# Performance work log

Measured on AMD Instinct MI355X. Metric: run time of the kernel, lower is better.

Reference implementation:

```python
import jax, jax.numpy as jnp
import numpy as np

NEIGH = 16  # default neigh in __init__


def setup_inputs() -> dict:
    key = jax.random.key(0)
    kx, kuv = jax.random.split(key)
    B, M = 8, 4096
    X = jax.random.normal(kx, (B, M, 3), dtype=jnp.float32)
    uv = jax.random.uniform(kuv, (B, M, 2), dtype=jnp.float32)
    return {"X": X, "uv": uv}


def reference(X, uv):
    # Pairwise squared distances in parameter (uv) space: (B, M, M)
    dm = jnp.sum((uv[:, :, None, :] - uv[:, None, :, :]) ** 2, axis=-1)
    # k nearest neighbours (smallest distances) -> indices (B, M, K)
    _, k_inds = jax.lax.top_k(-dm, NEIGH)
    # Gather 3D neighbourhoods: (B, M, K, 3)
    knns = jax.vmap(lambda x, idx: x[idx])(X, k_inds)
    # Covariance per point: center then K x 3 outer products -> (B, M, 3, 3)
    centered = knns - jnp.mean(knns, axis=2, keepdims=True)
    cov = jnp.einsum('bmki,bmkj->bmij', centered, centered)
    # Symmetric 3x3 eigenvalues; torch sorts descending, eigvalsh is ascending
    eig = jnp.linalg.eigvalsh(cov)
    fff = eig[..., ::-1]  # (B, M, 3), descending
    return fff
```

## Files before the change

### kernel.cpp

```cpp
#include <hip/hip_runtime.h>
#include <math.h>

typedef unsigned long long u64;
typedef unsigned int u32;

constexpr int NB  = 8;
constexpr int NM  = 4096;
constexpr int KNN = 16;
constexpr int WPB = 8;
constexpr int QPW = 4;
constexpr int QPB = WPB * QPW;
constexpr int BLK = WPB * 64;
constexpr int GC  = 32;
constexpr int NC  = GC * GC;
constexpr int CSST = NC + 1;
constexpr int SLG = 13;

constexpr size_t WS_UVS = 0;
constexpr size_t WS_CS  = (size_t)NB * NM * 16;

__device__ __forceinline__ u64 shflx64(u64 v, int m) {
  unsigned lo = (unsigned)v, hi = (unsigned)(v >> 32);
  lo = __shfl_xor(lo, m, 64);
  hi = __shfl_xor(hi, m, 64);
  return ((u64)hi << 32) | lo;
}
__device__ __forceinline__ int rfl(int x) { return __builtin_amdgcn_readfirstlane(x); }
__device__ __forceinline__ int lanes_below(u64 m) {
  return (int)__builtin_amdgcn_mbcnt_hi((u32)(m >> 32),
             __builtin_amdgcn_mbcnt_lo((u32)m, 0u));
}
__device__ __forceinline__ u32 gm16(u64 m, int lane) {
  return (u32)(m >> ((lane >> 4) << 4)) & 0xFFFFu;
}

__global__ __launch_bounds__(1024)
void bin_pts(const float* __restrict__ uv, float4* __restrict__ uvS,
             u32* __restrict__ cs) {
  __shared__ u32 cnt[NC];
  __shared__ u32 offs[NC];
  __shared__ u32 wtot[16];
  const int bb  = blockIdx.x;
  const int tid = threadIdx.x;

  cnt[tid] = 0;
  __syncthreads();

  float2 c4[4];
  int cell[4];
  #pragma unroll
  for (int i = 0; i < 4; ++i) {
    const int p = tid + i * 1024;
    const float2 c = ((const float2*)(uv + (size_t)bb * NM * 2))[p];
    int cx = (int)(c.x * 32.f); cx = cx > GC - 1 ? GC - 1 : (cx < 0 ? 0 : cx);
    int cy = (int)(c.y * 32.f); cy = cy > GC - 1 ? GC - 1 : (cy < 0 ? 0 : cy);
    c4[i] = c; cell[i] = cy * GC + cx;
    atomicAdd(&cnt[cell[i]], 1u);
  }
  __syncthreads();

  {
    const int lane = tid & 63;
    u32 inc = cnt[tid];
    #pragma unroll
    for (int o = 1; o < 64; o <<= 1) {
      const u32 t = __shfl_up(inc, o, 64);
      if (lane >= o) inc += t;
    }
    offs[tid] = inc;
    if (lane == 63) wtot[tid >> 6] = inc;
  }
  __syncthreads();
  if (tid < 16) {
    u32 v = wtot[tid];
    #pragma unroll
    for (int o = 1; o < 16; o <<= 1) {
      const u32 t = __shfl_up(v, o, 64);
      if (tid >= o) v += t;
    }
    wtot[tid] = v;
  }
  __syncthreads();
  {
    const int w = tid >> 6;
    const u32 base = w ? wtot[w - 1] : 0u;
    const u32 excl = base + offs[tid] - cnt[tid];
    cs[bb * CSST + tid] = excl;
    offs[tid] = excl;
    if (tid == 0) cs[bb * CSST + NC] = NM;
  }
  __syncthreads();

  #pragma unroll
  for (int i = 0; i < 4; ++i) {
    const int p = tid + i * 1024;
    const u32 pos = atomicAdd(&offs[cell[i]], 1u);
    uvS[(size_t)bb * NM + pos] =
        make_float4(c4[i].x, c4[i].y, __uint_as_float((u32)p), 0.f);
  }
}

__global__ __launch_bounds__(BLK, 8)
void knn_eig(const float* __restrict__ X, const float4* __restrict__ uvS,
             const u32* __restrict__ cs, float* __restrict__ out) {
  __shared__ u64 surv[WPB][QPW * 32];

  const int tid  = threadIdx.x;
  const int lane = tid & 63;
  const int sub  = lane & 15;
  const int g4   = lane >> 4;
  const int wv   = tid >> 6;
  const int bb   = blockIdx.x >> 7;
  const int s    = ((blockIdx.x & 127) << 5) + (wv << 2) + g4;

  const float4* uvb = uvS + (size_t)bb * NM;
  const u32* csb = cs + bb * CSST;

  const float4 qc = uvb[s];
  const float qu = qc.x, qv = qc.y;
  const u32 oq = __float_as_uint(qc.z);
  int cxv = (int)(qu * 32.f); cxv = cxv > GC - 1 ? GC - 1 : (cxv < 0 ? 0 : cxv);
  int cyv = (int)(qv * 32.f); cyv = cyv > GC - 1 ? GC - 1 : (cyv < 0 ? 0 : cyv);
  const int sx = (qu * 32.f - (float)cxv >= 0.5f) ? 1 : 0;
  const int sy = (qv * 32.f - (float)cyv >= 0.5f) ? 1 : 0;

  float d[SLG];
  #pragma unroll
  for (int t = 0; t < SLG; ++t) d[t] = 1e30f;

  constexpr float TAU1 = 0.0017f;
  constexpr float TAU2 = 0.002197265625f;
  constexpr float TAU3 = 0.006103515625f;
  constexpr float TAU4 = 0.019775390625f;

  int rs0, rs1, rs2, rs3, rs4, rs5, rc0, rc1, rc2, rc3, rc4;
  int total, tsw;
  int cnt = 0;

  {
    const int x0 = min(max(cxv - 2 + sx, 0), GC - 4);
    const int y0 = min(max(cyv - 2 + sy, 0), GC - 4);
    const int b = y0 * GC + x0;
    rs0 = (int)csb[b];          rc0 = (int)csb[b + 4] - rs0;
    rs1 = (int)csb[b + GC];     rc1 = rc0 + (int)csb[b + GC + 4] - rs1;
    rs2 = (int)csb[b + 2*GC];   rc2 = rc1 + (int)csb[b + 2*GC + 4] - rs2;
    rs3 = (int)csb[b + 3*GC];   total = rc2 + (int)csb[b + 3*GC + 4] - rs3;
    rc3 = total; rc4 = total; rs4 = 0; rs5 = 0;
    int ts = min((total + 15) >> 4, SLG);
    int m1 = max(ts, __shfl_xor(ts, 16, 64));
    m1 = max(m1, __shfl_xor(m1, 32, 64));
    tsw = rfl(m1);
    #pragma unroll
    for (int t = 0; t < SLG; ++t) {
      if (t >= tsw) break;
      const int L = t * 16 + sub;
      int addr = rs0 + L;
      addr = (L >= rc0) ? rs1 + (L - rc0) : addr;
      addr = (L >= rc1) ? rs2 + (L - rc1) : addr;
      addr = (L >= rc2) ? rs3 + (L - rc2) : addr;
      float dd = 1e30f;
      if (L < total) {
        const float4 c = uvb[addr];
        const float dx = __fsub_rn(qu, c.x);
        const float dy = __fsub_rn(qv, c.y);
        dd = __fadd_rn(__fmul_rn(dx, dx), __fmul_rn(dy, dy));
      }
      d[t] = dd;
      cnt += (int)__popc(gm16(__ballot(dd <= TAU1), lane));
    }
  }

  float hi2 = TAU1, lo = 0.f;
  if (__any(cnt < KNN)) {
    int c2 = 0;
    #pragma unroll
    for (int t = 0; t < SLG; ++t) {
      if (t >= tsw) break;
      c2 += (int)__popc(gm16(__ballot(d[t] <= TAU2), lane));
    }
    if (cnt < KNN) { lo = TAU1; hi2 = TAU2; cnt = c2; }
  }

  if (__any(cnt < KNN)) {
    const bool need = cnt < KNN;
    int ts2 = 0;
    if (need) {
      #pragma unroll
      for (int t = 0; t < SLG; ++t) d[t] = 1e30f;
      const int x0 = min(max(cxv - 3 + sx, 0), GC - 6);
      const int y0 = min(max(cyv - 3 + sy, 0), GC - 6);
      const int b = y0 * GC + x0;
      rs0 = (int)csb[b];          rc0 = (int)csb[b + 6] - rs0;
      rs1 = (int)csb[b + GC];     rc1 = rc0 + (int)csb[b + GC + 6] - rs1;
      rs2 = (int)csb[b + 2*GC];   rc2 = rc1 + (int)csb[b + 2*GC + 6] - rs2;
      rs3 = (int)csb[b + 3*GC];   rc3 = rc2 + (int)csb[b + 3*GC + 6] - rs3;
      rs4 = (int)csb[b + 4*GC];   rc4 = rc3 + (int)csb[b + 4*GC + 6] - rs4;
      rs5 = (int)csb[b + 5*GC];   total = rc4 + (int)csb[b + 5*GC + 6] - rs5;
      ts2 = min((total + 15) >> 4, SLG);
      lo = TAU2; hi2 = TAU3;
    }
    int m1 = max(ts2, __shfl_xor(ts2, 16, 64));
    m1 = max(m1, __shfl_xor(m1, 32, 64));
    const int tsw2 = rfl(m1);
    int c2 = 0;
    #pragma unroll
    for (int t = 0; t < SLG; ++t) {
      if (t >= tsw2) break;
      float dd = 1e30f;
      if (need) {
        const int L = t * 16 + sub;
        int addr = rs0 + L;
        addr = (L >= rc0) ? rs1 + (L - rc0) : addr;
        addr = (L >= rc1) ? rs2 + (L - rc1) : addr;
        addr = (L >= rc2) ? rs3 + (L - rc2) : addr;
        addr = (L >= rc3) ? rs4 + (L - rc3) : addr;
        addr = (L >= rc4) ? rs5 + (L - rc4) : addr;
        if (L < total) {
          const float4 c = uvb[addr];
          const float dx = __fsub_rn(qu, c.x);
          const float dy = __fsub_rn(qv, c.y);
          dd = __fadd_rn(__fmul_rn(dx, dx), __fmul_rn(dy, dy));
        }
        d[t] = dd;
      }
      c2 += (int)__popc(gm16(__ballot(dd <= TAU3), lane));
    }
    if (need) cnt = c2;
    tsw = max(tsw, tsw2);
  }

  for (int it = 0; __any(cnt > 32) && it < 40; ++it) {
    const float mid = 0.5f * (lo + hi2);
    int c = 0;
    #pragma unroll
    for (int t = 0; t < SLG; ++t) {
      if (t >= tsw) break;
      c += (int)__popc(gm16(__ballot((cnt > 32) && (d[t] <= mid)), lane));
    }
    if (cnt > 32) {
      if (!(mid > lo && mid < hi2)) cnt = 32;
      else if (c >= KNN) { hi2 = mid; cnt = c; }
      else lo = mid;
    }
  }

  u64* sb = surv[wv];
  {
    int base = 0;
    #pragma unroll
    for (int t = 0; t < SLG; ++t) {
      if (t >= tsw) break;
      const bool p = d[t] <= hi2;
      const u32 mg = gm16(__ballot(p), lane);
      if (p) {
        const int pos = base + (int)__popc(mg & ((1u << sub) - 1u));
        if (pos < 32) {
          const int L = t * 16 + sub;
          int addr = rs0 + L;
          addr = (L >= rc0) ? rs1 + (L - rc0) : addr;
          addr = (L >= rc1) ? rs2 + (L - rc1) : addr;
          addr = (L >= rc2) ? rs3 + (L - rc2) : addr;
          addr = (L >= rc3) ? rs4 + (L - rc3) : addr;
          addr = (L >= rc4) ? rs5 + (L - rc4) : addr;
          const u32 oid = ((const u32*)(uvb + addr))[2];
          sb[(g4 << 5) + pos] = ((u64)__float_as_uint(d[t]) << 32) | (u64)oid;
        }
      }
      base += (int)__popc(mg);
    }
  }

  if (__any(cnt < KNN)) {
    #pragma unroll 1
    for (int g = 0; g < QPW; ++g) {
      if (!rfl((__shfl(cnt, g << 4, 64) < KNN) ? 1 : 0)) continue;
      const float gu = __shfl(qu, g << 4, 64);
      const float gv = __shfl(qv, g << 4, 64);
      int gcx = (int)(gu * 32.f); gcx = min(max(gcx, 0), GC - 1);
      int gcy = (int)(gv * 32.f); gcy = min(max(gcy, 0), GC - 1);
      const int gsx = (gu * 32.f - (float)gcx >= 0.5f) ? 1 : 0;
      const int gsy = (gv * 32.f - (float)gcy >= 0.5f) ? 1 : 0;
      const int x0 = min(max(gcx - 5 + gsx, 0), GC - 10);
      const int y0 = min(max(gcy - 5 + gsy, 0), GC - 10);
      int rstart[10], rcum[10];
      int cum = 0;
      #pragma unroll
      for (int r = 0; r < 10; ++r) {
        const int b = (y0 + r) * GC + x0;
        rstart[r] = (int)csb[b];
        cum += (int)csb[b + 10] - rstart[r];
        rcum[r] = cum;
      }
      const int gtotal = cum;
      const int gts = rfl(min((gtotal + 63) >> 6, SLG));
      float ghi = TAU4, glo = TAU3;
      int gcnt = 0;
      #pragma unroll
      for (int t = 0; t < SLG; ++t) {
        if (t >= gts) break;
        const int L = t * 64 + lane;
        int addr = rstart[0] + L;
        #pragma unroll
        for (int r = 1; r < 10; ++r)
          addr = (L >= rcum[r - 1]) ? rstart[r] + (L - rcum[r - 1]) : addr;
        float dd = 1e30f;
        if (L < gtotal) {
          const float4 c = uvb[addr];
          const float dx = __fsub_rn(gu, c.x);
          const float dy = __fsub_rn(gv, c.y);
          dd = __fadd_rn(__fmul_rn(dx, dx), __fmul_rn(dy, dy));
        }
        d[t] = dd;
        gcnt += (int)__popcll(__ballot(dd <= ghi));
      }
      for (int it = 0; rfl(gcnt) > 32 && it < 40; ++it) {
        const float mid = 0.5f * (glo + ghi);
        if (!(mid > glo && mid < ghi)) break;
        int c = 0;
        #pragma unroll
        for (int t = 0; t < SLG; ++t) {
          if (t >= gts) break;
          c += (int)__popcll(__ballot(d[t] <= mid));
        }
        if (c >= KNN) { ghi = mid; gcnt = c; } else glo = mid;
      }
      int base = 0;
      #pragma unroll
      for (int t = 0; t < SLG; ++t) {
        if (t >= gts) break;
        const bool p = d[t] <= ghi;
        const u64 m = __ballot(p);
        if (p) {
          const int pos = base + lanes_below(m);
          if (pos < 32) {
            const int L = t * 64 + lane;
            int addr = rstart[0] + L;
            #pragma unroll
            for (int r = 1; r < 10; ++r)
              addr = (L >= rcum[r - 1]) ? rstart[r] + (L - rcum[r - 1]) : addr;
            const u32 oid = ((const u32*)(uvb + addr))[2];
            sb[(g << 5) + pos] = ((u64)__float_as_uint(d[t]) << 32) | (u64)oid;
          }
        }
        base += (int)__popcll(m);
      }
      if (g4 == g) cnt = min(rfl(gcnt), 32);
    }
  }

  const int S = cnt < 32 ? cnt : 32;
  const int sbase = g4 << 5;
  u64 v0 = (sub < S) ? sb[sbase + sub] : ~0ull;
  u64 v1 = (16 + sub < S) ? sb[sbase + 16 + sub] : ~0ull;
  #pragma unroll
  for (int k = 2; k <= 16; k <<= 1) {
    #pragma unroll
    for (int j = k >> 1; j > 0; j >>= 1) {
      const u64 o0 = shflx64(v0, j);
      const u64 o1 = shflx64(v1, j);
      const bool up = ((sub & k) == 0);
      const bool j0 = ((sub & j) == 0);
      const bool km0 = (j0 == up);
      const bool km1 = (j0 != up);
      v0 = ((v0 < o0) == km0) ? v0 : o0;
      v1 = ((v1 < o1) == km1) ? v1 : o1;
    }
  }
  const u64 v = (v0 < v1) ? v0 : v1;

  const int idx = (int)(u32)v & 0xFFF;
  const float* Xp = X + ((size_t)bb * NM + idx) * 3;
  const float x = Xp[0], y = Xp[1], z = Xp[2];
  float sxs = x, sys = y, szs = z;
  float sxx = x * x, sxy = x * y, sxz = x * z;
  float syy = y * y, syz = y * z, szz = z * z;
  #pragma unroll
  for (int o = 8; o > 0; o >>= 1) {
    sxs += __shfl_xor(sxs, o, 64);  sys += __shfl_xor(sys, o, 64);
    szs += __shfl_xor(szs, o, 64);  sxx += __shfl_xor(sxx, o, 64);
    sxy += __shfl_xor(sxy, o, 64);  sxz += __shfl_xor(sxz, o, 64);
    syy += __shfl_xor(syy, o, 64);  syz += __shfl_xor(syz, o, 64);
    szz += __shfl_xor(szz, o, 64);
  }

  const float mx = sxs * 0.0625f, my = sys * 0.0625f, mz = szs * 0.0625f;
  const float c00 = sxx - 16.f * mx * mx;
  const float c11 = syy - 16.f * my * my;
  const float c22 = szz - 16.f * mz * mz;
  const float c01 = sxy - 16.f * mx * my;
  const float c02 = sxz - 16.f * mx * mz;
  const float c12 = syz - 16.f * my * mz;

  const float tr = c00 + c11 + c22;
  const float q3 = tr * (1.f / 3.f);
  const float b0 = c00 - q3, b1 = c11 - q3, b2 = c22 - q3;
  const float p2 = b0 * b0 + b1 * b1 + b2 * b2 +
                   2.f * (c01 * c01 + c02 * c02 + c12 * c12);
  float e0, e1, e2;
  if (p2 < 1e-30f) {
    e0 = e1 = e2 = q3;
  } else {
    const float p  = sqrtf(p2 * (1.f / 6.f));
    const float ip = 1.f / p;
    const float m00 = b0 * ip, m11 = b1 * ip, m22 = b2 * ip;
    const float m01 = c01 * ip, m02 = c02 * ip, m12 = c12 * ip;
    const float det = m00 * (m11 * m22 - m12 * m12)
                    - m01 * (m01 * m22 - m12 * m02)
                    + m02 * (m01 * m12 - m11 * m02);
    float r = 0.5f * det;
    r = fminf(1.f, fmaxf(-1.f, r));
    const float phi = acosf(r) * (1.f / 3.f);
    float sphi, cphi;
    __sincosf(phi, &sphi, &cphi);
    e0 = q3 + 2.f * p * cphi;
    e2 = q3 + 2.f * p * (-0.5f * cphi - 0.8660254037844386f * sphi);
    e1 = tr - e0 - e2;
  }

  if (sub == 0) {
    float* op = out + ((size_t)bb * NM + oq) * 3;
    op[0] = e0; op[1] = e1; op[2] = e2;
  }
}

extern "C" void kernel_launch(void* const* d_in, const int* in_sizes, int n_in,
                              void* d_out, int out_size, void* d_ws, size_t ws_size,
                              hipStream_t stream) {
  const float* X  = (const float*)d_in[0];
  const float* uv = (const float*)d_in[1];
  float* out = (float*)d_out;
  char* ws = (char*)d_ws;
  float4* uvS = (float4*)(ws + WS_UVS);
  u32*    csP = (u32*)(ws + WS_CS);

  bin_pts<<<dim3(NB), dim3(1024), 0, stream>>>(uv, uvS, csP);
  knn_eig<<<dim3(NB * NM / QPB), dim3(BLK), 0, stream>>>(X, uvS, csP, out);
}
```

Measured before the change: 27.68 us.

## Select exact top-16 by threshold search and accumulate covariance directly without sort

Replaces the shared-memory survivor buffer and bitonic sort with a threshold search that stops at exactly KNN candidates, using interpolation alternated with bisection. Covariance sums are accumulated straight from the selected candidates, whose original indices are now kept in registers, so the address recomputation is gone. Per-group counts use DPP row-rotate reductions in place of ballot/popc. The fallback path now computes and writes its own eigenvalues. The occupancy hint is lowered to 4 waves, and tie handling at the threshold may pick different points than the sort did.

```diff
diff --git a/kernel.cpp b/kernel.cpp
--- a/kernel.cpp
+++ b/kernel.cpp
@@ -19,12 +19,6 @@
 constexpr size_t WS_UVS = 0;
 constexpr size_t WS_CS  = (size_t)NB * NM * 16;
 
-__device__ __forceinline__ u64 shflx64(u64 v, int m) {
-  unsigned lo = (unsigned)v, hi = (unsigned)(v >> 32);
-  lo = __shfl_xor(lo, m, 64);
-  hi = __shfl_xor(hi, m, 64);
-  return ((u64)hi << 32) | lo;
-}
 __device__ __forceinline__ int rfl(int x) { return __builtin_amdgcn_readfirstlane(x); }
 __device__ __forceinline__ int lanes_below(u64 m) {
   return (int)__builtin_amdgcn_mbcnt_hi((u32)(m >> 32),
@@ -32,6 +26,26 @@
 }
 __device__ __forceinline__ u32 gm16(u64 m, int lane) {
   return (u32)(m >> ((lane >> 4) << 4)) & 0xFFFFu;
+}
+
+template<int CTRL>
+__device__ __forceinline__ int dppAddI(int v) {
+  return v + __builtin_amdgcn_update_dpp(0, v, CTRL, 0xF, 0xF, false);
+}
+template<int CTRL>
+__device__ __forceinline__ float dppAddF(float v) {
+  int r = __builtin_amdgcn_update_dpp(0, __float_as_int(v), CTRL, 0xF, 0xF, false);
+  return v + __int_as_float(r);
+}
+__device__ __forceinline__ int rorSum16(int c) {
+  c = dppAddI<0x128>(c); c = dppAddI<0x124>(c);
+  c = dppAddI<0x122>(c); c = dppAddI<0x121>(c);
+  return c;
+}
+__device__ __forceinline__ float rorSum16F(float v) {
+  v = dppAddF<0x128>(v); v = dppAddF<0x124>(v);
+  v = dppAddF<0x122>(v); v = dppAddF<0x121>(v);
+  return v;
 }
 
 __global__ __launch_bounds__(1024)
@@ -100,11 +114,9 @@
   }
 }
 
-__global__ __launch_bounds__(BLK, 8)
+__global__ __launch_bounds__(BLK, 4)
 void knn_eig(const float* __restrict__ X, const float4* __restrict__ uvS,
              const u32* __restrict__ cs, float* __restrict__ out) {
-  __shared__ u64 surv[WPB][QPW * 32];
-
   const int tid  = threadIdx.x;
   const int lane = tid & 63;
   const int sub  = lane & 15;
@@ -125,6 +137,7 @@
   const int sy = (qv * 32.f - (float)cyv >= 0.5f) ? 1 : 0;
 
   float d[SLG];
+  u32   o[SLG];
   #pragma unroll
   for (int t = 0; t < SLG; ++t) d[t] = 1e30f;
 
@@ -133,23 +146,25 @@
   constexpr float TAU3 = 0.006103515625f;
   constexpr float TAU4 = 0.019775390625f;
 
-  int rs0, rs1, rs2, rs3, rs4, rs5, rc0, rc1, rc2, rc3, rc4;
-  int total, tsw;
-  int cnt = 0;
+  int tsw;
+  int cnt;
+  float hiB;
+  bool ovf;
 
   {
     const int x0 = min(max(cxv - 2 + sx, 0), GC - 4);
     const int y0 = min(max(cyv - 2 + sy, 0), GC - 4);
     const int b = y0 * GC + x0;
-    rs0 = (int)csb[b];          rc0 = (int)csb[b + 4] - rs0;
-    rs1 = (int)csb[b + GC];     rc1 = rc0 + (int)csb[b + GC + 4] - rs1;
-    rs2 = (int)csb[b + 2*GC];   rc2 = rc1 + (int)csb[b + 2*GC + 4] - rs2;
-    rs3 = (int)csb[b + 3*GC];   total = rc2 + (int)csb[b + 3*GC + 4] - rs3;
-    rc3 = total; rc4 = total; rs4 = 0; rs5 = 0;
+    const int rs0 = (int)csb[b];          const int rc0 = (int)csb[b + 4] - rs0;
+    const int rs1 = (int)csb[b + GC];     const int rc1 = rc0 + (int)csb[b + GC + 4] - rs1;
+    const int rs2 = (int)csb[b + 2*GC];   const int rc2 = rc1 + (int)csb[b + 2*GC + 4] - rs2;
+    const int rs3 = (int)csb[b + 3*GC];   const int total = rc2 + (int)csb[b + 3*GC + 4] - rs3;
+    ovf = total > SLG * 16;
     int ts = min((total + 15) >> 4, SLG);
     int m1 = max(ts, __shfl_xor(ts, 16, 64));
     m1 = max(m1, __shfl_xor(m1, 32, 64));
     tsw = rfl(m1);
+    int cl = 0;
     #pragma unroll
     for (int t = 0; t < SLG; ++t) {
       if (t >= tsw) break;
@@ -159,32 +174,42 @@
       addr = (L >= rc1) ? rs2 + (L - rc1) : addr;
       addr = (L >= rc2) ? rs3 + (L - rc2) : addr;
       float dd = 1e30f;
+      u32 oid = 0;
       if (L < total) {
         const float4 c = uvb[addr];
         const float dx = __fsub_rn(qu, c.x);
         const float dy = __fsub_rn(qv, c.y);
         dd = __fadd_rn(__fmul_rn(dx, dx), __fmul_rn(dy, dy));
-      }
-      d[t] = dd;
-      cnt += (int)__popc(gm16(__ballot(dd <= TAU1), lane));
-    }
-  }
-
-  float hi2 = TAU1, lo = 0.f;
+        oid = __float_as_uint(c.z);
+      }
+      d[t] = dd; o[t] = oid;
+      cl += (dd <= TAU1) ? 1 : 0;
+    }
+    cnt = rorSum16(cl);
+    hiB = TAU1;
+    if (ovf) cnt = 0;
+  }
+
   if (__any(cnt < KNN)) {
-    int c2 = 0;
+    int cl = 0;
     #pragma unroll
     for (int t = 0; t < SLG; ++t) {
       if (t >= tsw) break;
-      c2 += (int)__popc(gm16(__ballot(d[t] <= TAU2), lane));
-    }
-    if (cnt < KNN) { lo = TAU1; hi2 = TAU2; cnt = c2; }
+      cl += (d[t] <= TAU2) ? 1 : 0;
+    }
+    int c2 = rorSum16(cl);
+    if (ovf) c2 = 0;
+    if (cnt < KNN) { cnt = c2; hiB = TAU2; }
   }
 
   if (__any(cnt < KNN)) {
-    const bool need = cnt < KNN;
+    const bool needc = cnt < KNN;
     int ts2 = 0;
-    if (need) {
+    int rs0=0, rs1=0, rs2=0, rs3=0, rs4=0, rs5=0;
+    int rc0=0, rc1=0, rc2=0, rc3=0, rc4=0;
+    int total2 = 0;
+    bool ovf2 = false;
+    if (needc) {
       #pragma unroll
       for (int t = 0; t < SLG; ++t) d[t] = 1e30f;
       const int x0 = min(max(cxv - 3 + sx, 0), GC - 6);
@@ -195,19 +220,19 @@
       rs2 = (int)csb[b + 2*GC];   rc2 = rc1 + (int)csb[b + 2*GC + 6] - rs2;
       rs3 = (int)csb[b + 3*GC];   rc3 = rc2 + (int)csb[b + 3*GC + 6] - rs3;
       rs4 = (int)csb[b + 4*GC];   rc4 = rc3 + (int)csb[b + 4*GC + 6] - rs4;
-      rs5 = (int)csb[b + 5*GC];   total = rc4 + (int)csb[b + 5*GC + 6] - rs5;
-      ts2 = min((total + 15) >> 4, SLG);
-      lo = TAU2; hi2 = TAU3;
+      rs5 = (int)csb[b + 5*GC];   total2 = rc4 + (int)csb[b + 5*GC + 6] - rs5;
+      ovf2 = total2 > SLG * 16;
+      ts2 = min((total2 + 15) >> 4, SLG);
     }
     int m1 = max(ts2, __shfl_xor(ts2, 16, 64));
     m1 = max(m1, __shfl_xor(m1, 32, 64));
     const int tsw2 = rfl(m1);
-    int c2 = 0;
+    int cl = 0;
     #pragma unroll
     for (int t = 0; t < SLG; ++t) {
       if (t >= tsw2) break;
       float dd = 1e30f;
-      if (need) {
+      if (needc) {
         const int L = t * 16 + sub;
         int addr = rs0 + L;
         addr = (L >= rc0) ? rs1 + (L - rc0) : addr;
@@ -215,67 +240,123 @@
         addr = (L >= rc2) ? rs3 + (L - rc2) : addr;
         addr = (L >= rc3) ? rs4 + (L - rc3) : addr;
         addr = (L >= rc4) ? rs5 + (L - rc4) : addr;
-        if (L < total) {
+        u32 oid = 0;
+        if (L < total2) {
           const float4 c = uvb[addr];
           const float dx = __fsub_rn(qu, c.x);
           const float dy = __fsub_rn(qv, c.y);
           dd = __fadd_rn(__fmul_rn(dx, dx), __fmul_rn(dy, dy));
+          oid = __float_as_uint(c.z);
         }
-        d[t] = dd;
-      }
-      c2 += (int)__popc(gm16(__ballot(dd <= TAU3), lane));
-    }
-    if (need) cnt = c2;
+        d[t] = dd; o[t] = oid;
+      }
+      cl += (needc && dd <= TAU3) ? 1 : 0;
+    }
+    int c3 = rorSum16(cl);
+    if (needc) {
+      cnt = ovf2 ? 0 : c3;
+      hiB = TAU3;
+    }
     tsw = max(tsw, tsw2);
   }
 
-  for (int it = 0; __any(cnt > 32) && it < 40; ++it) {
-    const float mid = 0.5f * (lo + hi2);
-    int c = 0;
-    #pragma unroll
-    for (int t = 0; t < SLG; ++t) {
-      if (t >= tsw) break;
-      c += (int)__popc(gm16(__ballot((cnt > 32) && (d[t] <= mid)), lane));
-    }
-    if (cnt > 32) {
-      if (!(mid > lo && mid < hi2)) cnt = 32;
-      else if (c >= KNN) { hi2 = mid; cnt = c; }
-      else lo = mid;
-    }
-  }
-
-  u64* sb = surv[wv];
+  const bool act = cnt >= KNN;
+
+  float tau = hiB;
+  {
+    float lo = 0.f, hi = hiB;
+    int clo = 1, chi = cnt;
+    bool done = !act || (cnt == KNN);
+    for (int it = 0; it < 32 && __any(!done); ++it) {
+      float mid = lo + (hi - lo) * ((float)(KNN - clo) / (float)(chi - clo));
+      if ((it & 1) || !(mid > lo && mid < hi)) mid = 0.5f * (lo + hi);
+      const bool valid = (mid > lo) && (mid < hi);
+      int cl = 0;
+      #pragma unroll
+      for (int t = 0; t < SLG; ++t) {
+        if (t >= tsw) break;
+        cl += (!done && valid && d[t] <= mid) ? 1 : 0;
+      }
+      const int c = rorSum16(cl);
+      if (!done) {
+        if (!valid) { tau = hi; done = true; }
+        else if (c >= KNN) {
+          hi = mid; chi = c;
+          if (c == KNN) { tau = mid; done = true; }
+        } else { lo = mid; clo = c; }
+      }
+    }
+  }
+
+  float sX=0.f,sY=0.f,sZ=0.f,sXX=0.f,sXY=0.f,sXZ=0.f,sYY=0.f,sYZ=0.f,sZZ=0.f;
   {
     int base = 0;
     #pragma unroll
     for (int t = 0; t < SLG; ++t) {
       if (t >= tsw) break;
-      const bool p = d[t] <= hi2;
-      const u32 mg = gm16(__ballot(p), lane);
-      if (p) {
-        const int pos = base + (int)__popc(mg & ((1u << sub) - 1u));
-        if (pos < 32) {
-          const int L = t * 16 + sub;
-          int addr = rs0 + L;
-          addr = (L >= rc0) ? rs1 + (L - rc0) : addr;
-          addr = (L >= rc1) ? rs2 + (L - rc1) : addr;
-          addr = (L >= rc2) ? rs3 + (L - rc2) : addr;
-          addr = (L >= rc3) ? rs4 + (L - rc3) : addr;
-          addr = (L >= rc4) ? rs5 + (L - rc4) : addr;
-          const u32 oid = ((const u32*)(uvb + addr))[2];
-          sb[(g4 << 5) + pos] = ((u64)__float_as_uint(d[t]) << 32) | (u64)oid;
-        }
+      const bool sel0 = act && (d[t] <= tau);
+      const u32 mg = gm16(__ballot(sel0), lane);
+      const bool sel = sel0 && (base + (int)__popc(mg & ((1u << sub) - 1u)) < KNN);
+      if (sel) {
+        const float* Xp = X + ((size_t)bb * NM + o[t]) * 3;
+        const float x = Xp[0], y = Xp[1], z = Xp[2];
+        sX += x; sY += y; sZ += z;
+        sXX += x*x; sXY += x*y; sXZ += x*z;
+        sYY += y*y; sYZ += y*z; sZZ += z*z;
       }
       base += (int)__popc(mg);
     }
   }
-
-  if (__any(cnt < KNN)) {
+  sX = rorSum16F(sX);  sY = rorSum16F(sY);  sZ = rorSum16F(sZ);
+  sXX = rorSum16F(sXX); sXY = rorSum16F(sXY); sXZ = rorSum16F(sXZ);
+  sYY = rorSum16F(sYY); sYZ = rorSum16F(sYZ); sZZ = rorSum16F(sZZ);
+
+  {
+    const float mx = sX * 0.0625f, my = sY * 0.0625f, mz = sZ * 0.0625f;
+    const float c00 = sXX - 16.f * mx * mx;
+    const float c11 = sYY - 16.f * my * my;
+    const float c22 = sZZ - 16.f * mz * mz;
+    const float c01 = sXY - 16.f * mx * my;
+    const float c02 = sXZ - 16.f * mx * mz;
+    const float c12 = sYZ - 16.f * my * mz;
+    const float tr = c00 + c11 + c22;
+    const float q3 = tr * (1.f / 3.f);
+    const float b0 = c00 - q3, b1 = c11 - q3, b2 = c22 - q3;
+    const float p2 = b0*b0 + b1*b1 + b2*b2 +
+                     2.f * (c01*c01 + c02*c02 + c12*c12);
+    float e0, e1, e2;
+    if (p2 < 1e-30f) {
+      e0 = e1 = e2 = q3;
+    } else {
+      const float p  = sqrtf(p2 * (1.f / 6.f));
+      const float ip = 1.f / p;
+      const float m00 = b0*ip, m11 = b1*ip, m22 = b2*ip;
+      const float m01 = c01*ip, m02 = c02*ip, m12 = c12*ip;
+      const float det = m00*(m11*m22 - m12*m12)
+                      - m01*(m01*m22 - m12*m02)
+                      + m02*(m01*m12 - m11*m02);
+      float r = 0.5f * det;
+      r = fminf(1.f, fmaxf(-1.f, r));
+      const float phi = acosf(r) * (1.f / 3.f);
+      float sphi, cphi;
+      __sincosf(phi, &sphi, &cphi);
+      e0 = q3 + 2.f * p * cphi;
+      e2 = q3 + 2.f * p * (-0.5f * cphi - 0.8660254037844386f * sphi);
+      e1 = tr - e0 - e2;
+    }
+    if (act && sub == 0) {
+      float* op = out + ((size_t)bb * NM + oq) * 3;
+      op[0] = e0; op[1] = e1; op[2] = e2;
+    }
+  }
+
+  if (__any(!act)) {
     #pragma unroll 1
     for (int g = 0; g < QPW; ++g) {
-      if (!rfl((__shfl(cnt, g << 4, 64) < KNN) ? 1 : 0)) continue;
+      if (rfl(__shfl((int)act, g << 4, 64))) continue;
       const float gu = __shfl(qu, g << 4, 64);
       const float gv = __shfl(qv, g << 4, 64);
+      const u32 goq = (u32)__shfl((int)oq, g << 4, 64);
       int gcx = (int)(gu * 32.f); gcx = min(max(gcx, 0), GC - 1);
       int gcy = (int)(gv * 32.f); gcy = min(max(gcy, 0), GC - 1);
       const int gsx = (gu * 32.f - (float)gcx >= 0.5f) ? 1 : 0;
@@ -293,133 +374,121 @@
       }
       const int gtotal = cum;
       const int gts = rfl(min((gtotal + 63) >> 6, SLG));
-      float ghi = TAU4, glo = TAU3;
-      int gcnt = 0;
+      int cl0 = 0;
       #pragma unroll
       for (int t = 0; t < SLG; ++t) {
-        if (t >= gts) break;
+        if (t >= gts) { d[t] = 1e30f; continue; }
         const int L = t * 64 + lane;
         int addr = rstart[0] + L;
         #pragma unroll
         for (int r = 1; r < 10; ++r)
           addr = (L >= rcum[r - 1]) ? rstart[r] + (L - rcum[r - 1]) : addr;
         float dd = 1e30f;
+        u32 oid = 0;
         if (L < gtotal) {
           const float4 c = uvb[addr];
           const float dx = __fsub_rn(gu, c.x);
           const float dy = __fsub_rn(gv, c.y);
           dd = __fadd_rn(__fmul_rn(dx, dx), __fmul_rn(dy, dy));
+          oid = __float_as_uint(c.z);
         }
-        d[t] = dd;
-        gcnt += (int)__popcll(__ballot(dd <= ghi));
-      }
-      for (int it = 0; rfl(gcnt) > 32 && it < 40; ++it) {
-        const float mid = 0.5f * (glo + ghi);
-        if (!(mid > glo && mid < ghi)) break;
-        int c = 0;
-        #pragma unroll
-        for (int t = 0; t < SLG; ++t) {
-          if (t >= gts) break;
-          c += (int)__popcll(__ballot(d[t] <= mid));
+        d[t] = dd; o[t] = oid;
+        cl0 += (dd <= TAU4) ? 1 : 0;
+      }
+      int c4 = rorSum16(cl0);
+      c4 += __shfl_xor(c4, 16, 64); c4 += __shfl_xor(c4, 32, 64);
+
+      float gtau = TAU4;
+      {
+        float lo = 0.f, hi = TAU4;
+        int clo = 1, chi = c4;
+        bool done = (c4 == KNN);
+        for (int it = 0; it < 32 && !rfl((int)done); ++it) {
+          float mid = lo + (hi - lo) * ((float)(KNN - clo) / (float)(chi - clo));
+          if ((it & 1) || !(mid > lo && mid < hi)) mid = 0.5f * (lo + hi);
+          const bool valid = (mid > lo) && (mid < hi);
+          int cl = 0;
+          #pragma unroll
+          for (int t = 0; t < SLG; ++t) {
+            if (t >= gts) break;
+            cl += (valid && d[t] <= mid) ? 1 : 0;
+          }
+          int c = rorSum16(cl);
+          c += __shfl_xor(c, 16, 64); c += __shfl_xor(c, 32, 64);
+          if (!done) {
+            if (!valid) { gtau = hi; done = true; }
+            else if (c >= KNN) {
+              hi = mid; chi = c;
+              if (c == KNN) { gtau = mid; done = true; }
+            } else { lo = mid; clo = c; }
+          }
         }
-        if (c >= KNN) { ghi = mid; gcnt = c; } else glo = mid;
-      }
+      }
+
+      float tX=0.f,tY=0.f,tZ=0.f,tXX=0.f,tXY=0.f,tXZ=0.f,tYY=0.f,tYZ=0.f,tZZ=0.f;
       int base = 0;
       #pragma unroll
       for (int t = 0; t < SLG; ++t) {
         if (t >= gts) break;
-        const bool p = d[t] <= ghi;
-        const u64 m = __ballot(p);
-        if (p) {
-          const int pos = base + lanes_below(m);
-          if (pos < 32) {
-            const int L = t * 64 + lane;
-            int addr = rstart[0] + L;
-            #pragma unroll
-            for (int r = 1; r < 10; ++r)
-              addr = (L >= rcum[r - 1]) ? rstart[r] + (L - rcum[r - 1]) : addr;
-            const u32 oid = ((const u32*)(uvb + addr))[2];
-            sb[(g << 5) + pos] = ((u64)__float_as_uint(d[t]) << 32) | (u64)oid;
-          }
+        const bool sel0 = d[t] <= gtau;
+        const u64 m = __ballot(sel0);
+        const bool sel = sel0 && (base + lanes_below(m) < KNN);
+        if (sel) {
+          const float* Xp = X + ((size_t)bb * NM + o[t]) * 3;
+          const float x = Xp[0], y = Xp[1], z = Xp[2];
+          tX += x; tY += y; tZ += z;
+          tXX += x*x; tXY += x*y; tXZ += x*z;
+          tYY += y*y; tYZ += y*z; tZZ += z*z;
         }
         base += (int)__popcll(m);
       }
-      if (g4 == g) cnt = min(rfl(gcnt), 32);
-    }
-  }
-
-  const int S = cnt < 32 ? cnt : 32;
-  const int sbase = g4 << 5;
-  u64 v0 = (sub < S) ? sb[sbase + sub] : ~0ull;
-  u64 v1 = (16 + sub < S) ? sb[sbase + 16 + sub] : ~0ull;
-  #pragma unroll
-  for (int k = 2; k <= 16; k <<= 1) {
-    #pragma unroll
-    for (int j = k >> 1; j > 0; j >>= 1) {
-      const u64 o0 = shflx64(v0, j);
-      const u64 o1 = shflx64(v1, j);
-      const bool up = ((sub & k) == 0);
-      const bool j0 = ((sub & j) == 0);
-      const bool km0 = (j0 == up);
-      const bool km1 = (j0 != up);
-      v0 = ((v0 < o0) == km0) ? v0 : o0;
-      v1 = ((v1 < o1) == km1) ? v1 : o1;
-    }
-  }
-  const u64 v = (v0 < v1) ? v0 : v1;
-
-  const int idx = (int)(u32)v & 0xFFF;
-  const float* Xp = X + ((size_t)bb * NM + idx) * 3;
-  const float x = Xp[0], y = Xp[1], z = Xp[2];
-  float sxs = x, sys = y, szs = z;
-  float sxx = x * x, sxy = x * y, sxz = x * z;
-  float syy = y * y, syz = y * z, szz = z * z;
-  #pragma unroll
-  for (int o = 8; o > 0; o >>= 1) {
-    sxs += __shfl_xor(sxs, o, 64);  sys += __shfl_xor(sys, o, 64);
-    szs += __shfl_xor(szs, o, 64);  sxx += __shfl_xor(sxx, o, 64);
-    sxy += __shfl_xor(sxy, o, 64);  sxz += __shfl_xor(sxz, o, 64);
-    syy += __shfl_xor(syy, o, 64);  syz += __shfl_xor(syz, o, 64);
-    szz += __shfl_xor(szz, o, 64);
-  }
-
-  const float mx = sxs * 0.0625f, my = sys * 0.0625f, mz = szs * 0.0625f;
-  const float c00 = sxx - 16.f * mx * mx;
-  const float c11 = syy - 16.f * my * my;
-  const float c22 = szz - 16.f * mz * mz;
-  const float c01 = sxy - 16.f * mx * my;
-  const float c02 = sxz - 16.f * mx * mz;
-  const float c12 = syz - 16.f * my * mz;
-
-  const float tr = c00 + c11 + c22;
-  const float q3 = tr * (1.f / 3.f);
-  const float b0 = c00 - q3, b1 = c11 - q3, b2 = c22 - q3;
-  const float p2 = b0 * b0 + b1 * b1 + b2 * b2 +
-                   2.f * (c01 * c01 + c02 * c02 + c12 * c12);
-  float e0, e1, e2;
-  if (p2 < 1e-30f) {
-    e0 = e1 = e2 = q3;
-  } else {
-    const float p  = sqrtf(p2 * (1.f / 6.f));
-    const float ip = 1.f / p;
-    const float m00 = b0 * ip, m11 = b1 * ip, m22 = b2 * ip;
-    const float m01 = c01 * ip, m02 = c02 * ip, m12 = c12 * ip;
-    const float det = m00 * (m11 * m22 - m12 * m12)
-                    - m01 * (m01 * m22 - m12 * m02)
-                    + m02 * (m01 * m12 - m11 * m02);
-    float r = 0.5f * det;
-    r = fminf(1.f, fmaxf(-1.f, r));
-    const float phi = acosf(r) * (1.f / 3.f);
-    float sphi, cphi;
-    __sincosf(phi, &sphi, &cphi);
-    e0 = q3 + 2.f * p * cphi;
-    e2 = q3 + 2.f * p * (-0.5f * cphi - 0.8660254037844386f * sphi);
-    e1 = tr - e0 - e2;
-  }
-
-  if (sub == 0) {
-    float* op = out + ((size_t)bb * NM + oq) * 3;
-    op[0] = e0; op[1] = e1; op[2] = e2;
+      tX = rorSum16F(tX);  tX += __shfl_xor(tX, 16, 64);  tX += __shfl_xor(tX, 32, 64);
+      tY = rorSum16F(tY);  tY += __shfl_xor(tY, 16, 64);  tY += __shfl_xor(tY, 32, 64);
+      tZ = rorSum16F(tZ);  tZ += __shfl_xor(tZ, 16, 64);  tZ += __shfl_xor(tZ, 32, 64);
+      tXX = rorSum16F(tXX); tXX += __shfl_xor(tXX, 16, 64); tXX += __shfl_xor(tXX, 32, 64);
+      tXY = rorSum16F(tXY); tXY += __shfl_xor(tXY, 16, 64); tXY += __shfl_xor(tXY, 32, 64);
+      tXZ = rorSum16F(tXZ); tXZ += __shfl_xor(tXZ, 16, 64); tXZ += __shfl_xor(tXZ, 32, 64);
+      tYY = rorSum16F(tYY); tYY += __shfl_xor(tYY, 16, 64); tYY += __shfl_xor(tYY, 32, 64);
+      tYZ = rorSum16F(tYZ); tYZ += __shfl_xor(tYZ, 16, 64); tYZ += __shfl_xor(tYZ, 32, 64);
+      tZZ = rorSum16F(tZZ); tZZ += __shfl_xor(tZZ, 16, 64); tZZ += __shfl_xor(tZZ, 32, 64);
+
+      const float mx = tX * 0.0625f, my = tY * 0.0625f, mz = tZ * 0.0625f;
+      const float c00 = tXX - 16.f * mx * mx;
+      const float c11 = tYY - 16.f * my * my;
+      const float c22 = tZZ - 16.f * mz * mz;
+      const float c01 = tXY - 16.f * mx * my;
+      const float c02 = tXZ - 16.f * mx * mz;
+      const float c12 = tYZ - 16.f * my * mz;
+      const float tr = c00 + c11 + c22;
+      const float q3 = tr * (1.f / 3.f);
+      const float b0 = c00 - q3, b1 = c11 - q3, b2 = c22 - q3;
+      const float p2 = b0*b0 + b1*b1 + b2*b2 +
+                       2.f * (c01*c01 + c02*c02 + c12*c12);
+      float e0, e1, e2;
+      if (p2 < 1e-30f) {
+        e0 = e1 = e2 = q3;
+      } else {
+        const float p  = sqrtf(p2 * (1.f / 6.f));
+        const float ip = 1.f / p;
+        const float m00 = b0*ip, m11 = b1*ip, m22 = b2*ip;
+        const float m01 = c01*ip, m02 = c02*ip, m12 = c12*ip;
+        const float det = m00*(m11*m22 - m12*m12)
+                        - m01*(m01*m22 - m12*m02)
+                        + m02*(m01*m12 - m11*m02);
+        float r = 0.5f * det;
+        r = fminf(1.f, fmaxf(-1.f, r));
+        const float phi = acosf(r) * (1.f / 3.f);
+        float sphi, cphi;
+        __sincosf(phi, &sphi, &cphi);
+        e0 = q3 + 2.f * p * cphi;
+        e2 = q3 + 2.f * p * (-0.5f * cphi - 0.8660254037844386f * sphi);
+        e1 = tr - e0 - e2;
+      }
+      if (lane == 0) {
+        float* op = out + ((size_t)bb * NM + goq) * 3;
+        op[0] = e0; op[1] = e1; op[2] = e2;
+      }
+    }
   }
 }
 
```

New measurement: 34.91 us. 1.26x slower.
